# Kernel optimization log

Hardware: AMD Instinct MI355X
Metric: run time of the kernel (lower is better)

Reference implementation:

```python
import jax, jax.numpy as jnp
import numpy as np

NUM_INST = 32
EPS = 1e-5


def _conv(x, w, b, stride=1, pad=0):
    y = jax.lax.conv_general_dilated(
        x, w, (stride, stride), ((pad, pad), (pad, pad)),
        dimension_numbers=('NCHW', 'OIHW', 'NCHW'))
    return y + b[None, :, None, None]


def _deconv(x, w, b):
    # torch ConvTranspose2d(k=3, s=2, p=1, output_padding=1); w is (Cin, Cout, 3, 3)
    wf = jnp.flip(w, (2, 3)).transpose(1, 0, 2, 3)  # -> OIHW
    y = jax.lax.conv_general_dilated(
        x, wf, (1, 1), ((1, 2), (1, 2)), lhs_dilation=(2, 2),
        dimension_numbers=('NCHW', 'OIHW', 'NCHW'))
    return y + b[None, :, None, None]


def _inorm(x):
    m = x.mean((2, 3), keepdims=True)
    v = x.var((2, 3), keepdims=True)  # biased, matches InstanceNorm2d
    return (x - m) * jax.lax.rsqrt(v + EPS)


def _rpad(x, p=3):
    return jnp.pad(x, ((0, 0), (0, 0), (p, p), (p, p)), mode='reflect')


def _backbone(input, w0, b0, w1, b1, w2, b2, w3, b3, w4, b4,
              w5, b5, w6, b6, w7, b7, w8, b8, w9, b9):
    x = jax.nn.relu(_inorm(_conv(_rpad(input), w0, b0)))          # [B,16,H,W]
    x = jax.nn.relu(_inorm(_conv(x, w1, b1, stride=2, pad=1)))    # [B,32,H/2,..]
    x = jax.nn.relu(_inorm(_conv(x, w2, b2, stride=2, pad=1)))    # [B,64,H/4,..]
    x = jax.nn.relu(_inorm(_conv(x, w3, b3, stride=2, pad=1)))    # [B,128,H/8,..]
    x = jax.nn.relu(_inorm(_conv(x, w4, b4, stride=2, pad=1)))    # [B,256,H/16,..]
    x = jax.nn.relu(_inorm(_deconv(x, w5, b5)))                   # [B,128,H/8,..]
    x = jax.nn.relu(_inorm(_deconv(x, w6, b6)))                   # [B,64,H/4,..]
    x = jax.nn.relu(_inorm(_deconv(x, w7, b7)))                   # [B,32,H/2,..]
    x = jax.nn.relu(_inorm(_deconv(x, w8, b8)))                   # [B,16,H,W]
    return jnp.tanh(_conv(_rpad(x), w9, b9))                      # [B,Cout,H,W]


def _segment_mean(outputs, inst):
    # outputs [B,C,H,W]; inst [B,1,H,W] int labels shared across the batch.
    B, C, H, W = outputs.shape
    seg = inst.reshape(-1)                                # [B*H*W]
    feats = outputs.transpose(0, 2, 3, 1).reshape(-1, C)  # [B*H*W, C]
    sums = jax.ops.segment_sum(feats, seg, num_segments=NUM_INST)
    counts = jax.ops.segment_sum(jnp.ones((feats.shape[0],), feats.dtype), seg,
                                 num_segments=NUM_INST)
    means = sums / jnp.maximum(counts, 1.0)[:, None]      # [NUM_INST, C]
    out = means[seg].reshape(B, H, W, C).transpose(0, 3, 1, 2)
    return out


def setup_inputs() -> dict:
    key = jax.random.key(0)
    ks = jax.random.split(key, 16)
    B, Cin, Cout, H, W = 4, 3, 3, 512, 512
    inp = {
        'input': jax.random.normal(ks[0], (B, Cin, H, W), jnp.float32),
        'inst': jax.random.randint(ks[1], (B, 1, H, W), 0, NUM_INST, jnp.int32),
    }
    std = 0.02
    # conv weights OIHW; deconv weights torch-style (Cin, Cout, kH, kW)
    shapes = [
        ('w0', (16, Cin, 7, 7)), ('w1', (32, 16, 3, 3)), ('w2', (64, 32, 3, 3)),
        ('w3', (128, 64, 3, 3)), ('w4', (256, 128, 3, 3)),
        ('w5', (256, 128, 3, 3)), ('w6', (128, 64, 3, 3)),
        ('w7', (64, 32, 3, 3)), ('w8', (32, 16, 3, 3)), ('w9', (Cout, 16, 7, 7)),
    ]
    bias_dims = [16, 32, 64, 128, 256, 128, 64, 32, 16, Cout]
    for i, (name, shp) in enumerate(shapes):
        inp[name] = std * jax.random.normal(ks[2 + i], shp, jnp.float32)
        inp['b%d' % i] = jnp.zeros((bias_dims[i],), jnp.float32)
    return inp


def reference(input, inst, w0, b0, w1, b1, w2, b2, w3, b3, w4, b4,
              w5, b5, w6, b6, w7, b7, w8, b8, w9, b9):
    outputs = _backbone(input, w0, b0, w1, b1, w2, b2, w3, b3, w4, b4,
                        w5, b5, w6, b6, w7, b7, w8, b8, w9, b9)
    return _segment_mean(outputs, inst)
```

## Files before the change

kernel.cpp:

```cpp
#include <hip/hip_runtime.h>
#include <math.h>

#define EPS_F 1e-5f

typedef __attribute__((ext_vector_type(8))) short short8;
typedef __attribute__((ext_vector_type(4))) float f32x4;
typedef __attribute__((ext_vector_type(8))) unsigned short ushort8;

__device__ __forceinline__ int reflect512(int v) {
    v = v < 0 ? -v : v;
    return v >= 512 ? 1022 - v : v;
}

__device__ __forceinline__ ushort f2bf(float f) {
    union { float f; unsigned u; } v; v.f = f;
    unsigned r = v.u + 0x7FFFu + ((v.u >> 16) & 1u);
    return (ushort)(r >> 16);
}
__device__ __forceinline__ float bf2f(ushort u) {
    union { unsigned u; float f; } v; v.u = (unsigned)u << 16;
    return v.f;
}

__device__ __forceinline__ float fast_tanh(float x) {
    float cx = fminf(fmaxf(x, -9.f), 9.f);
    float e  = __builtin_amdgcn_exp2f(cx * 2.8853900817779268f);
    return (e - 1.f) * __builtin_amdgcn_rcpf(e + 1.f);
}

template<int CIN, int COUT, bool DEC>
__device__ __forceinline__ void wp_mid(
    const float* __restrict__ w, ushort* __restrict__ dst, int i)
{
    constexpr int CIP = ((CIN + 31) / 32) * 32;
    int ci = i % CIP;
    int oc = (i / CIP) % COUT;
    int t  = i / (CIP * COUT);
    float x = 0.f;
    if (ci < CIN)
        x = DEC ? w[((size_t)ci * COUT + oc) * 9 + t]
                : w[((size_t)oc * CIN + ci) * 9 + t];
    dst[i] = f2bf(x);
}

__device__ __forceinline__ void wp_l1(
    const float* __restrict__ w, ushort* __restrict__ dst, int i)
{
    int k  = i & 31;
    int oc = (i >> 5) & 31;
    int c  = i >> 10;
    int tapsel = k >> 4, ci = k & 15;
    int t = 2 * c + tapsel;
    float x = (t < 9) ? w[((size_t)oc * 16 + ci) * 9 + t] : 0.f;
    dst[i] = f2bf(x);
}

template<bool L9>
__device__ __forceinline__ void wp_7(
    const float* __restrict__ w, ushort* __restrict__ dst, int i)
{
    int j   = i & 7;
    int oc  = (i >> 3) & 15;
    int kqe = (i >> 7) & 3;
    int cn  = i >> 9;
    float x = 0.f;
    if (L9) {
        int k = kqe * 8 + j;
        int tapsel = k >> 4, ci = k & 15;
        int ty = cn >> 2, q = cn & 3;
        int tx = 2 * q + tapsel;
        if (tx < 7 && oc < 3 && ty < 7)
            x = w[((size_t)oc * 16 + ci) * 49 + ty * 7 + tx];
    } else {
        int k = cn * 32 + kqe * 8 + j;
        int t = k >> 3, ci = k & 7;
        if (t < 49 && ci < 3)
            x = w[((size_t)oc * 3 + ci) * 49 + t];
    }
    dst[i] = f2bf(x);
}

struct WprepArgs {
    const float* w[10];
    ushort* d[10];
};

__global__ __launch_bounds__(256) void wprep_all(WprepArgs a)
{
    int bi = blockIdx.x;
    int t  = threadIdx.x;
    if      (bi < 20)   wp_l1(a.w[1], a.d[1], (bi        ) * 256 + t);
    else if (bi < 92)   wp_mid<32,  64,  false>(a.w[2], a.d[2], (bi - 20   ) * 256 + t);
    else if (bi < 380)  wp_mid<64,  128, false>(a.w[3], a.d[3], (bi - 92   ) * 256 + t);
    else if (bi < 1532) wp_mid<128, 256, false>(a.w[4], a.d[4], (bi - 380  ) * 256 + t);
    else if (bi < 2684) wp_mid<256, 128, true >(a.w[5], a.d[5], (bi - 1532 ) * 256 + t);
    else if (bi < 2972) wp_mid<128, 64,  true >(a.w[6], a.d[6], (bi - 2684 ) * 256 + t);
    else if (bi < 3044) wp_mid<64,  32,  true >(a.w[7], a.d[7], (bi - 2972 ) * 256 + t);
    else if (bi < 3062) wp_mid<32,  16,  true >(a.w[8], a.d[8], (bi - 3044 ) * 256 + t);
    else if (bi < 3088) wp_7<false>(a.w[0], a.d[0], (bi - 3062) * 256 + t);
    else                wp_7<true >(a.w[9], a.d[9], (bi - 3088) * 256 + t);
}

template<int CIN, int COUT, int WIN, int MODE, int NWN, int MSUB, int RT, int CT>
__global__ __launch_bounds__(256) void mfconv(
    const ushort* __restrict__ in, const ushort* __restrict__ wbf,
    const float* __restrict__ bias, ushort* __restrict__ out,
    const float* __restrict__ stats_in, float invHWin,
    float* __restrict__ stats_out)
{
    constexpr int HWIN = WIN * WIN;
    constexpr int WOUT = (MODE == 0) ? (WIN / 2) : (WIN * 2);
    constexpr int HWOUT = WOUT * WOUT;
    constexpr int NMG = 4 / NWN;
    constexpr int NOC = NWN * 16;
    constexpr int M = NMG * MSUB * 16;
    static_assert(M == RT * CT, "tile mismatch");
    constexpr int SPAN = (MODE == 0) ? WOUT : WIN;
    constexpr int XC = SPAN / CT, YC = SPAN / RT;
    constexpr int NG = COUT / NOC;
    constexpr int NR = (MODE == 0) ? (2 * RT + 1) : (RT + 1);
    constexpr int NCO = (MODE == 0) ? (2 * CT + 1) : (CT + 1);
    constexpr int NPIX = NR * NCO;
    constexpr int CIP = ((CIN + 31) / 32) * 32;
    constexpr int NQ = (MODE == 0) ? 1 : 4;
    constexpr int LPW = 36;
    constexpr int NPOUT = (MODE == 0 ? 1 : 4) * M;
    constexpr int NOCP = NOC + 8;

    constexpr int TDY[9] = {1,1,1,0,0,0,0,0,0};
    constexpr int TDX[9] = {1,0,0,1,0,0,1,0,0};
    constexpr int TQ [9] = {3,2,3,1,0,1,3,2,3};

    extern __shared__ ushort sa[];
    __shared__ float mrall[CIP][2];
    __shared__ float sred[4][16][2];

    const int tid = threadIdx.x;
    const int lane = tid & 63, wv = tid >> 6;
    const int ln = lane & 15, kq = lane >> 4;
    const int wn = wv % NWN, wm = wv / NWN;
    const int grp = tid & 3;

    int bi = blockIdx.x;
    const int xc = bi % XC; bi /= XC;
    const int yc = bi % YC; bi /= YC;
    const int g  = bi % NG;
    const int b  = bi / NG;

    const int ocg = g * NOC + wn * 16 + ln;
    const float b0 = bias[ocg];
    f32x4 acc[NQ][MSUB];
    #pragma unroll
    for (int q = 0; q < NQ; q++)
        #pragma unroll
        for (int s = 0; s < MSUB; s++)
            acc[q][s] = (f32x4){b0, b0, b0, b0};

    for (int e = tid; e < CIP; e += 256) {
        float m = 0.f, r = 0.f;
        if (e < CIN) {
            int c = b * CIN + e;
            float s1 = stats_in[2 * c], s2 = stats_in[2 * c + 1];
            m = s1 * invHWin;
            r = rsqrtf(fmaf(s2, invHWin, -m * m) + EPS_F);
        }
        mrall[e][0] = m; mrall[e][1] = r;
    }

    const ushort* inb = in + (size_t)b * HWIN * CIN;

    for (int c0 = 0; c0 < CIP; c0 += 32) {
        __syncthreads();
        const int ch0 = c0 + 8 * grp;
        float m8[8], r8[8];
        #pragma unroll
        for (int j = 0; j < 8; j++) { m8[j] = mrall[ch0 + j][0]; r8[j] = mrall[ch0 + j][1]; }
        for (int pix = tid >> 2; pix < NPIX; pix += 64) {
            int pr = pix / NCO, pc = pix - pr * NCO;
            int gy, gx;
            if (MODE == 0) { gy = 2 * (yc * RT) - 1 + pr; gx = 2 * (xc * CT) - 1 + pc; }
            else           { gy = yc * RT + pr;           gx = xc * CT + pc; }
            ushort8 pk;
            #pragma unroll
            for (int j = 0; j < 8; j++) pk[j] = 0;
            if ((unsigned)gy < (unsigned)WIN && (unsigned)gx < (unsigned)WIN && ch0 < CIN) {
                ushort8 raw = *(const ushort8*)(inb + (size_t)(gy * WIN + gx) * CIN + ch0);
                #pragma unroll
                for (int j = 0; j < 8; j++) {
                    float x = bf2f(raw[j]);
                    pk[j] = f2bf(fmaxf((x - m8[j]) * r8[j], 0.f));
                }
            }
            *(ushort8*)&sa[pix * LPW + grp * 8] = pk;
        }
        __syncthreads();
        #pragma unroll
        for (int t = 0; t < 9; t++) {
            short8 bfr = *(const short8*)&wbf[((size_t)t * COUT + ocg) * CIP + c0 + kq * 8];
            #pragma unroll
            for (int s = 0; s < MSUB; s++) {
                const int mb = wm * MSUB * 16 + s * 16;
                const int r = mb / CT, cb = mb % CT;
                int pix;
                if (MODE == 0) pix = (t / 3 + 2 * r) * NCO + 2 * (cb + ln) + t % 3;
                else           pix = (TDY[t] + r) * NCO + cb + ln + TDX[t];
                short8 afr = *(const short8*)&sa[pix * LPW + kq * 8];
                int qd = (MODE == 0) ? 0 : TQ[t];
                acc[qd][s] = __builtin_amdgcn_mfma_f32_16x16x32_bf16(afr, bfr, acc[qd][s], 0, 0, 0);
            }
        }
    }

    float s1 = 0.f, s2 = 0.f;
    #pragma unroll
    for (int q = 0; q < NQ; q++)
        #pragma unroll
        for (int s = 0; s < MSUB; s++)
            #pragma unroll
            for (int rg = 0; rg < 4; rg++) {
                float v = acc[q][s][rg];
                s1 += v; s2 = fmaf(v, v, s2);
            }
    s1 += __shfl_xor(s1, 16); s2 += __shfl_xor(s2, 16);
    s1 += __shfl_xor(s1, 32); s2 += __shfl_xor(s2, 32);
    if (lane < 16) { sred[wv][lane][0] = s1; sred[wv][lane][1] = s2; }

    __syncthreads();
    const int ocl = wn * 16 + ln;
    if (MODE == 0) {
        #pragma unroll
        for (int s = 0; s < MSUB; s++)
            #pragma unroll
            for (int rg = 0; rg < 4; rg++) {
                const int m = wm * MSUB * 16 + s * 16 + kq * 4 + rg;
                sa[m * NOCP + ocl] = f2bf(acc[0][s][rg]);
            }
    } else {
        #pragma unroll
        for (int q = 0; q < 4; q++) {
            const int dy = q >> 1, dx = q & 1;
            #pragma unroll
            for (int s = 0; s < MSUB; s++)
                #pragma unroll
                for (int rg = 0; rg < 4; rg++) {
                    const int m = wm * MSUB * 16 + s * 16 + kq * 4 + rg;
                    const int r = m / CT, c = m % CT;
                    const int lp = (2 * r + dy) * (2 * CT) + 2 * c + dx;
                    sa[lp * NOCP + ocl] = f2bf(acc[q][s][rg]);
                }
        }
    }
    __syncthreads();

    ushort* ob = out + (size_t)b * HWOUT * COUT + g * NOC;
    for (int e = tid; e < (NPOUT * NOC) / 8; e += 256) {
        int u = e * 8;
        int lp = u / NOC, co = u % NOC;
        int gp;
        if (MODE == 0) {
            int r = lp / CT, c = lp % CT;
            gp = (yc * RT + r) * WOUT + xc * CT + c;
        } else {
            int r2 = lp / (2 * CT), x2 = lp % (2 * CT);
            gp = (2 * (yc * RT) + r2) * WOUT + 2 * (xc * CT) + x2;
        }
        *(ushort8*)&ob[(size_t)gp * COUT + co] = *(const ushort8*)&sa[lp * NOCP + co];
    }

    if (tid < NOC) {
        int wnn = tid >> 4, oc = tid & 15;
        float t1 = 0.f, t2 = 0.f;
        #pragma unroll
        for (int k = 0; k < NMG; k++) {
            t1 += sred[wnn + k * NWN][oc][0];
            t2 += sred[wnn + k * NWN][oc][1];
        }
        int cix = b * COUT + g * NOC + wnn * 16 + oc;
        atomicAdd(&stats_out[2 * cix],     t1);
        atomicAdd(&stats_out[2 * cix + 1], t2);
    }
}

__global__ __launch_bounds__(256) void mfconv_l1(
    const ushort* __restrict__ in, const ushort* __restrict__ wbf,
    const float* __restrict__ bias, ushort* __restrict__ out,
    const float* __restrict__ stats_in, float invHWin,
    float* __restrict__ stats_out)
{
    constexpr int WIN = 512, HWIN = WIN * WIN;
    constexpr int WOUT = 256, HWOUT = WOUT * WOUT;
    constexpr int COUT = 32, RT = 4, CT = 32;
    constexpr int NCO = 65, NPIX = 585;
    constexpr int LPW = 20;
    constexpr int NOCP = 40;

    extern __shared__ ushort sa[];
    __shared__ float mrall[16][2];
    __shared__ float sred[4][16][2];

    const int tid = threadIdx.x;
    const int lane = tid & 63, wv = tid >> 6;
    const int ln = lane & 15, kq = lane >> 4;
    const int wn = wv & 1, wm = wv >> 1;

    int bi = blockIdx.x;
    const int xc = bi & 7;
    const int yc = (bi >> 3) & 63;
    const int b  = bi >> 9;

    const int ocg = wn * 16 + ln;
    const float b0 = bias[ocg];
    f32x4 acc[4];
    #pragma unroll
    for (int s = 0; s < 4; s++) acc[s] = (f32x4){b0, b0, b0, b0};

    if (tid < 16) {
        int c = b * 16 + tid;
        float s1 = stats_in[2 * c], s2 = stats_in[2 * c + 1];
        float m = s1 * invHWin;
        mrall[tid][0] = m;
        mrall[tid][1] = rsqrtf(fmaf(s2, invHWin, -m * m) + EPS_F);
    }

    const int grp = tid & 1, p0 = tid >> 1;
    const ushort* inb = in + (size_t)b * HWIN * 16 + grp * 8;
    ushort8 rw[5];
    bool ok[5];
    #pragma unroll
    for (int i = 0; i < 5; i++) {
        int pix = p0 + i * 128;
        int pr = pix / NCO, pc = pix - pr * NCO;
        int gy = 2 * (yc * RT) - 1 + pr;
        int gx = 2 * (xc * CT) - 1 + pc;
        ok[i] = (pix < NPIX) && ((unsigned)gy < (unsigned)WIN)
                             && ((unsigned)gx < (unsigned)WIN);
        if (ok[i])
            rw[i] = *(const ushort8*)(inb + (size_t)(gy * WIN + gx) * 16);
    }
    __syncthreads();

    float m8[8], r8[8];
    #pragma unroll
    for (int j = 0; j < 8; j++) {
        m8[j] = mrall[grp * 8 + j][0];
        r8[j] = mrall[grp * 8 + j][1];
    }
    #pragma unroll
    for (int i = 0; i < 5; i++) {
        int pix = p0 + i * 128;
        if (pix < NPIX) {
            ushort8 pk;
            #pragma unroll
            for (int j = 0; j < 8; j++) pk[j] = 0;
            if (ok[i]) {
                #pragma unroll
                for (int j = 0; j < 8; j++) {
                    float x = bf2f(rw[i][j]);
                    pk[j] = f2bf(fmaxf((x - m8[j]) * r8[j], 0.f));
                }
            }
            *(ushort8*)&sa[pix * LPW + grp * 8] = pk;
        }
    }
    __syncthreads();

    const int tp = kq >> 1, off8 = (kq & 1) * 8;
    #pragma unroll
    for (int c = 0; c < 5; c++) {
        short8 bfr = *(const short8*)&wbf[(size_t)(c * COUT + ocg) * 32 + kq * 8];
        int t = 2 * c + tp; t = t > 8 ? 8 : t;
        const int ty = t / 3, tx = t - 3 * ty;
        #pragma unroll
        for (int s = 0; s < 4; s++) {
            const int mb = wm * 64 + s * 16;
            const int r = mb >> 5, cb = mb & 31;
            short8 afr = *(const short8*)
                &sa[((ty + 2 * r) * NCO + 2 * (cb + ln) + tx) * LPW + off8];
            acc[s] = __builtin_amdgcn_mfma_f32_16x16x32_bf16(afr, bfr, acc[s], 0, 0, 0);
        }
    }

    float s1 = 0.f, s2 = 0.f;
    #pragma unroll
    for (int s = 0; s < 4; s++)
        #pragma unroll
        for (int rg = 0; rg < 4; rg++) {
            float v = acc[s][rg];
            s1 += v; s2 = fmaf(v, v, s2);
        }
    s1 += __shfl_xor(s1, 16); s2 += __shfl_xor(s2, 16);
    s1 += __shfl_xor(s1, 32); s2 += __shfl_xor(s2, 32);
    if (lane < 16) { sred[wv][lane][0] = s1; sred[wv][lane][1] = s2; }

    __syncthreads();
    const int ocl = wn * 16 + ln;
    #pragma unroll
    for (int s = 0; s < 4; s++)
        #pragma unroll
        for (int rg = 0; rg < 4; rg++) {
            const int m = wm * 64 + s * 16 + kq * 4 + rg;
            sa[m * NOCP + ocl] = f2bf(acc[s][rg]);
        }
    __syncthreads();
    ushort* ob = out + (size_t)b * HWOUT * COUT;
    for (int e = tid; e < 512; e += 256) {
        int u = e * 8;
        int lp = u >> 5, co = u & 31;
        int r = lp >> 5, c = lp & 31;
        int gp = (yc * RT + r) * WOUT + xc * CT + c;
        *(ushort8*)&ob[(size_t)gp * COUT + co] = *(const ushort8*)&sa[lp * NOCP + co];
    }
    if (tid < 32) {
        int wnn = tid >> 4, oc = tid & 15;
        float t1 = 0.f, t2 = 0.f;
        #pragma unroll
        for (int k = 0; k < 2; k++) {
            t1 += sred[wnn + k * 2][oc][0];
            t2 += sred[wnn + k * 2][oc][1];
        }
        int cix = b * COUT + wnn * 16 + oc;
        atomicAdd(&stats_out[2 * cix],     t1);
        atomicAdd(&stats_out[2 * cix + 1], t2);
    }
}

template<bool BFIN, bool SEG>
__global__ __launch_bounds__(256, 4) void conv7x(
    const float* __restrict__ inf, const ushort* __restrict__ inb16,
    const ushort* __restrict__ wpk, const float* __restrict__ bias,
    ushort* __restrict__ out,
    const float* __restrict__ stats_in, float invHWin,
    float* __restrict__ stats_out,
    const int* __restrict__ inst, float* __restrict__ segacc)
{
    constexpr int W = 512, HW = 512 * 512;
    constexpr int STR = BFIN ? 20 : 12;
    constexpr int SASZ = BFIN ? (980 * 20 + 16) : 12288;

    __shared__ ushort sa[SASZ];
    __shared__ float mr[16][2];
    __shared__ float segl[SEG ? 128 : 1];
    __shared__ float sred[4][16][2];

    const int tid = threadIdx.x;
    const int lane = tid & 63, wv = tid >> 6;
    const int ln = lane & 15, kq = lane >> 4;

    int bi = blockIdx.x;
    const int xc = bi & 7;
    const int yr = (bi >> 3) & 63;
    const int b  = bi >> 9;
    const int y0 = yr * 8, x0 = xc * 64;

    if constexpr (SEG) { if (tid < 128) segl[tid] = 0.f; }
    if constexpr (BFIN) {
        if (tid < 16) {
            int c = b * 16 + tid;
            float s1 = stats_in[2 * c], s2 = stats_in[2 * c + 1];
            float m = s1 * invHWin;
            mr[tid][0] = m;
            mr[tid][1] = rsqrtf(fmaf(s2, invHWin, -m * m) + EPS_F);
        }
        if (tid >= 32 && tid < 48) sa[980 * 20 + (tid - 32)] = 0;
        __syncthreads();
        const int h = tid & 1;
        float m8[8], r8[8];
        #pragma unroll
        for (int j = 0; j < 8; j++) { m8[j] = mr[8 * h + j][0]; r8[j] = mr[8 * h + j][1]; }
        const ushort* inb = inb16 + (size_t)b * HW * 16;
        for (int pix = tid >> 1; pix < 980; pix += 128) {
            int pr = pix / 70, pc = pix - pr * 70;
            int gy = reflect512(y0 - 3 + pr);
            int gx = reflect512(x0 - 3 + pc);
            ushort8 raw = *(const ushort8*)(inb + (size_t)(gy * W + gx) * 16 + 8 * h);
            ushort8 pk;
            #pragma unroll
            for (int j = 0; j < 8; j++) {
                float x = bf2f(raw[j]);
                pk[j] = f2bf(fmaxf((x - m8[j]) * r8[j], 0.f));
            }
            *(ushort8*)&sa[pix * STR + 8 * h] = pk;
        }
    } else {
        const float* p0 = inf + (size_t)b * 3 * HW;
        for (int pix = tid; pix < 980; pix += 256) {
            int pr = pix / 70, pc = pix - pr * 70;
            int gy = reflect512(y0 - 3 + pr);
            int gx = reflect512(x0 - 3 + pc);
            const float* p = p0 + gy * W + gx;
            ushort8 pk;
            #pragma unroll
            for (int j = 0; j < 8; j++) pk[j] = 0;
            pk[0] = f2bf(p[0]); pk[1] = f2bf(p[HW]); pk[2] = f2bf(p[2 * (size_t)HW]);
            *(ushort8*)&sa[pix * STR] = pk;
        }
    }
    __syncthreads();

    const float b0 = (ln < (BFIN ? 3 : 16)) ? bias[ln] : 0.f;
    f32x4 acc[8];
    #pragma unroll
    for (int s = 0; s < 8; s++) acc[s] = (f32x4){b0, b0, b0, b0};

    if constexpr (BFIN) {
        const int c0 = wv * 16;
        const int abase = (c0 + ln + (kq >> 1)) * STR + (kq & 1) * 8;
        const ushort* wp9 = wpk + ((size_t)kq * 16 + ln) * 8;
        #pragma unroll
        for (int q = 0; q < 4; q++) {
            short8 bw[7];
            #pragma unroll
            for (int ty = 0; ty < 7; ty++)
                bw[ty] = *(const short8*)(wp9 + (size_t)(ty * 4 + q) * 512);
            #pragma unroll
            for (int r = 0; r < 14; r++) {
                short8 afr = *(const short8*)&sa[abase + q * (2 * STR) + r * (70 * STR)];
                #pragma unroll
                for (int ty = 0; ty < 7; ty++) {
                    const int s = r - ty;
                    if (s >= 0 && s < 8)
                        acc[s] = __builtin_amdgcn_mfma_f32_16x16x32_bf16(afr, bw[ty], acc[s], 0, 0, 0);
                }
            }
        }
    } else {
        for (int cn = 0; cn < 13; cn++) {
            short8 bfr = *(const short8*)&wpk[((size_t)(cn * 4 + kq) * 16 + ln) * 8];
            int t = 4 * cn + kq;
            t = t > 48 ? 48 : t;
            const int ty = t / 7, tx = t - ty * 7;
            #pragma unroll
            for (int s = 0; s < 8; s++) {
                int m = wv * 128 + s * 16 + ln;
                int r = m >> 6, c = m & 63;
                short8 afr = *(const short8*)&sa[((r + ty) * 70 + c + tx) * STR];
                acc[s] = __builtin_amdgcn_mfma_f32_16x16x32_bf16(afr, bfr, acc[s], 0, 0, 0);
            }
        }
    }

    if constexpr (SEG) {
        float* sf = (float*)sa;
        __syncthreads();
        if (ln < 3) {
            #pragma unroll
            for (int s = 0; s < 8; s++)
                #pragma unroll
                for (int rg = 0; rg < 4; rg++) {
                    int m = s * 64 + wv * 16 + kq * 4 + rg;
                    sf[m * 5 + ln] = acc[s][rg];
                }
        }
        __syncthreads();
        const int* ib = inst + ((size_t)b << 18);
        for (int p2 = tid; p2 < 512; p2 += 256) {
            int r = p2 >> 6, c = p2 & 63;
            int lab = ib[(y0 + r) * W + x0 + c] & 31;
            atomicAdd(&segl[lab * 4 + 0], fast_tanh(sf[p2 * 5 + 0]));
            atomicAdd(&segl[lab * 4 + 1], fast_tanh(sf[p2 * 5 + 1]));
            atomicAdd(&segl[lab * 4 + 2], fast_tanh(sf[p2 * 5 + 2]));
            atomicAdd(&segl[lab * 4 + 3], 1.f);
        }
        __syncthreads();
        if (tid < 128) {
            float v = segl[tid];
            if (v != 0.f) atomicAdd(&segacc[tid], v);
        }
    } else {
        float s1 = 0.f, s2 = 0.f;
        #pragma unroll
        for (int s = 0; s < 8; s++)
            #pragma unroll
            for (int rg = 0; rg < 4; rg++) {
                float v = acc[s][rg];
                s1 += v; s2 = fmaf(v, v, s2);
            }
        s1 += __shfl_xor(s1, 16); s2 += __shfl_xor(s2, 16);
        s1 += __shfl_xor(s1, 32); s2 += __shfl_xor(s2, 32);
        if (lane < 16) { sred[wv][lane][0] = s1; sred[wv][lane][1] = s2; }

        __syncthreads();
        #pragma unroll
        for (int s = 0; s < 8; s++)
            #pragma unroll
            for (int rg = 0; rg < 4; rg++) {
                int m = wv * 128 + s * 16 + kq * 4 + rg;
                sa[m * 24 + ln] = f2bf(acc[s][rg]);
            }
        __syncthreads();
        ushort* ob = out + (size_t)b * HW * 16;
        for (int e = tid; e < 1024; e += 256) {
            int u = e * 8;
            int lp = u >> 4, co = u & 15;
            int gp = (y0 + (lp >> 6)) * W + x0 + (lp & 63);
            *(ushort8*)&ob[(size_t)gp * 16 + co] = *(const ushort8*)&sa[lp * 24 + co];
        }
        if (tid < 16) {
            float t1 = 0.f, t2 = 0.f;
            #pragma unroll
            for (int k = 0; k < 4; k++) { t1 += sred[k][tid][0]; t2 += sred[k][tid][1]; }
            int cix = b * 16 + tid;
            atomicAdd(&stats_out[2 * cix],     t1);
            atomicAdd(&stats_out[2 * cix + 1], t2);
        }
    }
}

#define HW9 262144
__global__ void seg_final(const float* __restrict__ acc, float* __restrict__ means)
{
    int i = threadIdx.x;
    if (i < 96) {
        int s = i / 3, c = i - s * 3;
        means[i] = acc[s * 4 + c] / fmaxf(acc[s * 4 + 3], 1.f);
    }
}

__global__ __launch_bounds__(256) void seg_scatter(
    const int* __restrict__ inst, const float* __restrict__ means,
    float* __restrict__ out)
{
    int p   = blockIdx.x * 256 + threadIdx.x;
    int b   = p >> 18;
    int r   = p & (HW9 - 1);
    int lab = inst[p] & 31;
    float* ob = out + (size_t)b * 3 * HW9;
    ob[r]           = means[lab * 3 + 0];
    ob[HW9 + r]     = means[lab * 3 + 1];
    ob[2 * HW9 + r] = means[lab * 3 + 2];
}

extern "C" void kernel_launch(void* const* d_in, const int* in_sizes, int n_in,
                              void* d_out, int out_size, void* d_ws, size_t ws_size,
                              hipStream_t stream)
{
    const float* x_in = (const float*)d_in[0];
    const int*   inst = (const int*)d_in[1];
    const float* W_[10];
    const float* Bs[10];
    for (int i = 0; i < 10; i++) {
        W_[i] = (const float*)d_in[2 + 2 * i];
        Bs[i] = (const float*)d_in[3 + 2 * i];
    }
    float* out = (float*)d_out;

    ushort* Ab  = (ushort*)d_ws;
    ushort* Bb2 = Ab + (size_t)16777216;
    float*  st  = (float*)(Bb2 + (size_t)8388608);
    const int coff[9] = {0, 128, 384, 896, 1920, 3968, 4992, 5504, 5760};
    float* s_[9];
    for (int i = 0; i < 9; i++) s_[i] = st + coff[i];
    float* segacc = st + 5888;
    float* means  = st + 6016;
    ushort* wb = (ushort*)(st + 8192);
    const size_t OW1 = 0, OW2 = 9216, OW3 = 27648, OW4 = 101376,
                 OW5 = 396288, OW6 = 691200, OW7 = 764928, OW8 = 783360;
    ushort* wb0 = wb + 790000;
    ushort* wb9 = wb0 + 6656;

    hipMemsetAsync(st, 0, 6016 * sizeof(float), stream);

    WprepArgs wa;
    for (int i = 0; i < 10; i++) wa.w[i] = W_[i];
    wa.d[0] = wb0;
    wa.d[1] = wb + OW1; wa.d[2] = wb + OW2; wa.d[3] = wb + OW3; wa.d[4] = wb + OW4;
    wa.d[5] = wb + OW5; wa.d[6] = wb + OW6; wa.d[7] = wb + OW7; wa.d[8] = wb + OW8;
    wa.d[9] = wb9;
    wprep_all<<<dim3(3144), dim3(256), 0, stream>>>(wa);

    conv7x<false, false><<<dim3(2048), dim3(256), 0, stream>>>(
        x_in, nullptr, wb0, Bs[0], Ab, nullptr, 0.f, s_[0], nullptr, nullptr);

    mfconv_l1<<<dim3(2048), dim3(256), 23400, stream>>>(
        Ab, wb + OW1, Bs[1], Bb2, s_[0], 1.f / 262144.f, s_[1]);

    mfconv<32, 64, 256, 0, 2, 4, 4, 32><<<dim3(1024), dim3(256), 42120, stream>>>(
        Bb2, wb + OW2, Bs[2], Ab, s_[1], 1.f / 65536.f, s_[2]);

    mfconv<64, 128, 128, 0, 2, 4, 4, 32><<<dim3(512), dim3(256), 42120, stream>>>(
        Ab, wb + OW3, Bs[3], Bb2, s_[2], 1.f / 16384.f, s_[3]);

    mfconv<128, 256, 64, 0, 2, 2, 2, 32><<<dim3(512), dim3(256), 23400, stream>>>(
        Bb2, wb + OW4, Bs[4], Ab, s_[3], 1.f / 4096.f, s_[4]);

    mfconv<256, 128, 32, 1, 1, 1, 2, 32><<<dim3(512), dim3(256), 12288, stream>>>(
        Ab, wb + OW5, Bs[5], Bb2, s_[4], 1.f / 1024.f, s_[5]);

    mfconv<128, 64, 64, 1, 2, 2, 2, 32><<<dim3(512), dim3(256), 20480, stream>>>(
        Bb2, wb + OW6, Bs[6], Ab, s_[5], 1.f / 4096.f, s_[6]);

    mfconv<64, 32, 128, 1, 2, 2, 2, 32><<<dim3(1024), dim3(256), 20480, stream>>>(
        Ab, wb + OW7, Bs[7], Bb2, s_[6], 1.f / 16384.f, s_[7]);

    mfconv<32, 16, 256, 1, 1, 2, 2, 64><<<dim3(2048), dim3(256), 24576, stream>>>(
        Bb2, wb + OW8, Bs[8], Ab, s_[7], 1.f / 65536.f, s_[8]);

    conv7x<true, true><<<dim3(2048), dim3(256), 0, stream>>>(
        nullptr, Ab, wb9, Bs[9], nullptr, s_[8], 1.f / 262144.f, nullptr, inst, segacc);

    seg_final<<<dim3(1), dim3(96), 0, stream>>>(segacc, means);
    seg_scatter<<<dim3(4096), dim3(256), 0, stream>>>(inst, means, out);
}
```

Baseline: 481.7 us.

## Restructure 7x7 convs: row-tap MFMA reuse for first layer, smaller tiles and sharded seg atomics

The first 7x7 conv now packs input as 4-channel pixels and uses row-wise weight fragments, so each A fragment loaded from LDS is reused across 7 kernel rows, in place of the earlier 13-step im2col gather. The last conv switches to 32-column tiles with a 2x2 wave layout and twice as many blocks, which should improve occupancy and load balance. Segment-sum atomics are spread over 8 copies of the accumulator to reduce contention, and seg_final sums the copies. This adds extra halo loads for the smaller tiles and a larger memset.

```diff
diff --git a/kernel.cpp b/kernel.cpp
--- a/kernel.cpp
+++ b/kernel.cpp
@@ -6,6 +6,7 @@
 typedef __attribute__((ext_vector_type(8))) short short8;
 typedef __attribute__((ext_vector_type(4))) float f32x4;
 typedef __attribute__((ext_vector_type(8))) unsigned short ushort8;
+typedef __attribute__((ext_vector_type(4))) unsigned short ushort4v;
 
 __device__ __forceinline__ int reflect512(int v) {
     v = v < 0 ? -v : v;
@@ -72,10 +73,10 @@
         if (tx < 7 && oc < 3 && ty < 7)
             x = w[((size_t)oc * 16 + ci) * 49 + ty * 7 + tx];
     } else {
-        int k = cn * 32 + kqe * 8 + j;
-        int t = k >> 3, ci = k & 7;
-        if (t < 49 && ci < 3)
-            x = w[((size_t)oc * 3 + ci) * 49 + t];
+        int k = kqe * 8 + j;
+        int dx = k >> 2, ci = k & 3;
+        if (dx < 7 && ci < 3)
+            x = w[((size_t)oc * 3 + ci) * 49 + cn * 7 + dx];
     }
     dst[i] = f2bf(x);
 }
@@ -97,8 +98,8 @@
     else if (bi < 2972) wp_mid<128, 64,  true >(a.w[6], a.d[6], (bi - 2684 ) * 256 + t);
     else if (bi < 3044) wp_mid<64,  32,  true >(a.w[7], a.d[7], (bi - 2972 ) * 256 + t);
     else if (bi < 3062) wp_mid<32,  16,  true >(a.w[8], a.d[8], (bi - 3044 ) * 256 + t);
-    else if (bi < 3088) wp_7<false>(a.w[0], a.d[0], (bi - 3062) * 256 + t);
-    else                wp_7<true >(a.w[9], a.d[9], (bi - 3088) * 256 + t);
+    else if (bi < 3076) wp_7<false>(a.w[0], a.d[0], (bi - 3062) * 256 + t);
+    else                wp_7<true >(a.w[9], a.d[9], (bi - 3076) * 256 + t);
 }
 
 template<int CIN, int COUT, int WIN, int MODE, int NWN, int MSUB, int RT, int CT>
@@ -434,8 +435,13 @@
     const int* __restrict__ inst, float* __restrict__ segacc)
 {
     constexpr int W = 512, HW = 512 * 512;
-    constexpr int STR = BFIN ? 20 : 12;
-    constexpr int SASZ = BFIN ? (980 * 20 + 16) : 12288;
+    constexpr int TCOL = BFIN ? 32 : 64;
+    constexpr int HCOL = TCOL + 6;
+    constexpr int NPIXH = 14 * HCOL;
+    constexpr int STR = BFIN ? 20 : 4;
+    constexpr int SASZ = BFIN ? (532 * 20 + 40) : 12288;
+    constexpr int XCN = 512 / TCOL;
+    constexpr int NS = BFIN ? 4 : 8;
 
     __shared__ ushort sa[SASZ];
     __shared__ float mr[16][2];
@@ -447,10 +453,10 @@
     const int ln = lane & 15, kq = lane >> 4;
 
     int bi = blockIdx.x;
-    const int xc = bi & 7;
-    const int yr = (bi >> 3) & 63;
-    const int b  = bi >> 9;
-    const int y0 = yr * 8, x0 = xc * 64;
+    const int xc = bi % XCN;
+    const int yr = (bi / XCN) & 63;
+    const int b  = bi / (XCN * 64);
+    const int y0 = yr * 8, x0 = xc * TCOL;
 
     if constexpr (SEG) { if (tid < 128) segl[tid] = 0.f; }
     if constexpr (BFIN) {
@@ -461,15 +467,15 @@
             mr[tid][0] = m;
             mr[tid][1] = rsqrtf(fmaf(s2, invHWin, -m * m) + EPS_F);
         }
-        if (tid >= 32 && tid < 48) sa[980 * 20 + (tid - 32)] = 0;
+        if (tid >= 64 && tid < 104) sa[532 * 20 + (tid - 64)] = 0;
         __syncthreads();
         const int h = tid & 1;
         float m8[8], r8[8];
         #pragma unroll
         for (int j = 0; j < 8; j++) { m8[j] = mr[8 * h + j][0]; r8[j] = mr[8 * h + j][1]; }
         const ushort* inb = inb16 + (size_t)b * HW * 16;
-        for (int pix = tid >> 1; pix < 980; pix += 128) {
-            int pr = pix / 70, pc = pix - pr * 70;
+        for (int pix = tid >> 1; pix < NPIXH; pix += 128) {
+            int pr = pix / HCOL, pc = pix - pr * HCOL;
             int gy = reflect512(y0 - 3 + pr);
             int gx = reflect512(x0 - 3 + pc);
             ushort8 raw = *(const ushort8*)(inb + (size_t)(gy * W + gx) * 16 + 8 * h);
@@ -483,28 +489,28 @@
         }
     } else {
         const float* p0 = inf + (size_t)b * 3 * HW;
-        for (int pix = tid; pix < 980; pix += 256) {
-            int pr = pix / 70, pc = pix - pr * 70;
+        for (int pix = tid; pix < NPIXH; pix += 256) {
+            int pr = pix / HCOL, pc = pix - pr * HCOL;
             int gy = reflect512(y0 - 3 + pr);
             int gx = reflect512(x0 - 3 + pc);
             const float* p = p0 + gy * W + gx;
-            ushort8 pk;
-            #pragma unroll
-            for (int j = 0; j < 8; j++) pk[j] = 0;
-            pk[0] = f2bf(p[0]); pk[1] = f2bf(p[HW]); pk[2] = f2bf(p[2 * (size_t)HW]);
-            *(ushort8*)&sa[pix * STR] = pk;
-        }
+            ushort4v pk;
+            pk[0] = f2bf(p[0]); pk[1] = f2bf(p[HW]);
+            pk[2] = f2bf(p[2 * (size_t)HW]); pk[3] = 0;
+            *(ushort4v*)&sa[pix * 4] = pk;
+        }
+        if (tid < 16) sa[980 * 4 + tid] = 0;
     }
     __syncthreads();
 
     const float b0 = (ln < (BFIN ? 3 : 16)) ? bias[ln] : 0.f;
-    f32x4 acc[8];
-    #pragma unroll
-    for (int s = 0; s < 8; s++) acc[s] = (f32x4){b0, b0, b0, b0};
+    f32x4 acc[NS];
+    #pragma unroll
+    for (int s = 0; s < NS; s++) acc[s] = (f32x4){b0, b0, b0, b0};
 
     if constexpr (BFIN) {
-        const int c0 = wv * 16;
-        const int abase = (c0 + ln + (kq >> 1)) * STR + (kq & 1) * 8;
+        const int wr = wv >> 1, wc = wv & 1;
+        const int abase = ((wr * 4) * HCOL + wc * 16 + ln + (kq >> 1)) * STR + (kq & 1) * 8;
         const ushort* wp9 = wpk + ((size_t)kq * 16 + ln) * 8;
         #pragma unroll
         for (int q = 0; q < 4; q++) {
@@ -513,48 +519,54 @@
             for (int ty = 0; ty < 7; ty++)
                 bw[ty] = *(const short8*)(wp9 + (size_t)(ty * 4 + q) * 512);
             #pragma unroll
-            for (int r = 0; r < 14; r++) {
-                short8 afr = *(const short8*)&sa[abase + q * (2 * STR) + r * (70 * STR)];
+            for (int rr = 0; rr < 10; rr++) {
+                short8 afr = *(const short8*)&sa[abase + q * (2 * STR) + rr * (HCOL * STR)];
                 #pragma unroll
                 for (int ty = 0; ty < 7; ty++) {
-                    const int s = r - ty;
-                    if (s >= 0 && s < 8)
+                    const int s = rr - ty;
+                    if (s >= 0 && s < 4)
                         acc[s] = __builtin_amdgcn_mfma_f32_16x16x32_bf16(afr, bw[ty], acc[s], 0, 0, 0);
                 }
             }
         }
     } else {
-        for (int cn = 0; cn < 13; cn++) {
-            short8 bfr = *(const short8*)&wpk[((size_t)(cn * 4 + kq) * 16 + ln) * 8];
-            int t = 4 * cn + kq;
-            t = t > 48 ? 48 : t;
-            const int ty = t / 7, tx = t - ty * 7;
-            #pragma unroll
-            for (int s = 0; s < 8; s++) {
-                int m = wv * 128 + s * 16 + ln;
-                int r = m >> 6, c = m & 63;
-                short8 afr = *(const short8*)&sa[((r + ty) * 70 + c + tx) * STR];
-                acc[s] = __builtin_amdgcn_mfma_f32_16x16x32_bf16(afr, bfr, acc[s], 0, 0, 0);
+        const int c0 = wv * 16;
+        const int abase = (c0 + ln + 2 * kq) * 4;
+        const ushort* wp0 = wpk + ((size_t)kq * 16 + ln) * 8;
+        short8 bw[7];
+        #pragma unroll
+        for (int ty = 0; ty < 7; ty++)
+            bw[ty] = *(const short8*)(wp0 + (size_t)ty * 512);
+        #pragma unroll
+        for (int R = 0; R < 14; R++) {
+            short8 afr = *(const short8*)&sa[abase + R * (HCOL * 4)];
+            #pragma unroll
+            for (int ty = 0; ty < 7; ty++) {
+                const int s = R - ty;
+                if (s >= 0 && s < 8)
+                    acc[s] = __builtin_amdgcn_mfma_f32_16x16x32_bf16(afr, bw[ty], acc[s], 0, 0, 0);
             }
         }
     }
 
     if constexpr (SEG) {
+        const int wr = wv >> 1, wc = wv & 1;
         float* sf = (float*)sa;
         __syncthreads();
         if (ln < 3) {
             #pragma unroll
-            for (int s = 0; s < 8; s++)
+            for (int s = 0; s < 4; s++)
                 #pragma unroll
                 for (int rg = 0; rg < 4; rg++) {
-                    int m = s * 64 + wv * 16 + kq * 4 + rg;
+                    int m = (wr * 4 + s) * 32 + wc * 16 + kq * 4 + rg;
                     sf[m * 5 + ln] = acc[s][rg];
                 }
         }
         __syncthreads();
         const int* ib = inst + ((size_t)b << 18);
-        for (int p2 = tid; p2 < 512; p2 += 256) {
-            int r = p2 >> 6, c = p2 & 63;
+        {
+            int p2 = tid;
+            int r = p2 >> 5, c = p2 & 31;
             int lab = ib[(y0 + r) * W + x0 + c] & 31;
             atomicAdd(&segl[lab * 4 + 0], fast_tanh(sf[p2 * 5 + 0]));
             atomicAdd(&segl[lab * 4 + 1], fast_tanh(sf[p2 * 5 + 1]));
@@ -564,12 +576,13 @@
         __syncthreads();
         if (tid < 128) {
             float v = segl[tid];
-            if (v != 0.f) atomicAdd(&segacc[tid], v);
+            if (v != 0.f)
+                atomicAdd(&segacc[(blockIdx.x & 7) * 128 + tid], v);
         }
     } else {
         float s1 = 0.f, s2 = 0.f;
         #pragma unroll
-        for (int s = 0; s < 8; s++)
+        for (int s = 0; s < NS; s++)
             #pragma unroll
             for (int rg = 0; rg < 4; rg++) {
                 float v = acc[s][rg];
@@ -584,7 +597,7 @@
         for (int s = 0; s < 8; s++)
             #pragma unroll
             for (int rg = 0; rg < 4; rg++) {
-                int m = wv * 128 + s * 16 + kq * 4 + rg;
+                int m = s * 64 + wv * 16 + kq * 4 + rg;
                 sa[m * 24 + ln] = f2bf(acc[s][rg]);
             }
         __syncthreads();
@@ -612,7 +625,13 @@
     int i = threadIdx.x;
     if (i < 96) {
         int s = i / 3, c = i - s * 3;
-        means[i] = acc[s * 4 + c] / fmaxf(acc[s * 4 + 3], 1.f);
+        float num = 0.f, den = 0.f;
+        #pragma unroll
+        for (int k = 0; k < 8; k++) {
+            num += acc[k * 128 + s * 4 + c];
+            den += acc[k * 128 + s * 4 + 3];
+        }
+        means[i] = num / fmaxf(den, 1.f);
     }
 }
 
@@ -651,14 +670,14 @@
     float* s_[9];
     for (int i = 0; i < 9; i++) s_[i] = st + coff[i];
     float* segacc = st + 5888;
-    float* means  = st + 6016;
+    float* means  = st + 6912;
     ushort* wb = (ushort*)(st + 8192);
     const size_t OW1 = 0, OW2 = 9216, OW3 = 27648, OW4 = 101376,
                  OW5 = 396288, OW6 = 691200, OW7 = 764928, OW8 = 783360;
     ushort* wb0 = wb + 790000;
     ushort* wb9 = wb0 + 6656;
 
-    hipMemsetAsync(st, 0, 6016 * sizeof(float), stream);
+    hipMemsetAsync(st, 0, 6912 * sizeof(float), stream);
 
     WprepArgs wa;
     for (int i = 0; i < 10; i++) wa.w[i] = W_[i];
@@ -666,7 +685,7 @@
     wa.d[1] = wb + OW1; wa.d[2] = wb + OW2; wa.d[3] = wb + OW3; wa.d[4] = wb + OW4;
     wa.d[5] = wb + OW5; wa.d[6] = wb + OW6; wa.d[7] = wb + OW7; wa.d[8] = wb + OW8;
     wa.d[9] = wb9;
-    wprep_all<<<dim3(3144), dim3(256), 0, stream>>>(wa);
+    wprep_all<<<dim3(3132), dim3(256), 0, stream>>>(wa);
 
     conv7x<false, false><<<dim3(2048), dim3(256), 0, stream>>>(
         x_in, nullptr, wb0, Bs[0], Ab, nullptr, 0.f, s_[0], nullptr, nullptr);
@@ -695,7 +714,7 @@
     mfconv<32, 16, 256, 1, 1, 2, 2, 64><<<dim3(2048), dim3(256), 24576, stream>>>(
         Bb2, wb + OW8, Bs[8], Ab, s_[7], 1.f / 65536.f, s_[8]);
 
-    conv7x<true, true><<<dim3(2048), dim3(256), 0, stream>>>(
+    conv7x<true, true><<<dim3(4096), dim3(256), 0, stream>>>(
         nullptr, Ab, wb9, Bs[9], nullptr, s_[8], 1.f / 262144.f, nullptr, inst, segacc);
 
     seg_final<<<dim3(1), dim3(96), 0, stream>>>(segacc, means);
```

Measured after the change: 459.0 us. -4.7%, faster.
